# Kernel tuning notes

Measured on AMD Instinct MI355X. Metric: run time of the kernel, lower is better.

The kernel has to match this reference:

```python
import jax, jax.numpy as jnp
import numpy as np

N = 40000        # total nodes (2000 graphs x 20 nodes)
E = 60000        # edges per relation (before self-loops)
R = 6            # number of relations
IN = 32
HID = 128
OUT = 128
H = 2            # heads
C = 128          # per-head out channels (concat=False)
B = 2000         # number of graphs
NEG_SLOPE = 0.2


def setup_inputs() -> dict:
    key = jax.random.key(0)
    ks = jax.random.split(key, 16)
    rn = lambda k, s, sc=0.05: (jax.random.normal(k, s, jnp.float32) * sc)
    x = jax.random.normal(ks[0], (N, IN), jnp.float32)
    edge_index = jax.random.randint(ks[1], (R, 2, E), 0, N, dtype=jnp.int32)
    batch = (jnp.arange(N, dtype=jnp.int32) // (N // B)).astype(jnp.int32)
    return {
        "x": x, "edge_index": edge_index, "batch": batch,
        "Wl1": rn(ks[2], (R, IN, H * C)), "bl1": jnp.zeros((R, H * C), jnp.float32),
        "Wr1": rn(ks[3], (R, IN, H * C)), "br1": jnp.zeros((R, H * C), jnp.float32),
        "att1": rn(ks[4], (R, H, C)), "bias1": jnp.zeros((R, C), jnp.float32),
        "Wl2": rn(ks[5], (R, HID, H * C)), "bl2": jnp.zeros((R, H * C), jnp.float32),
        "Wr2": rn(ks[6], (R, HID, H * C)), "br2": jnp.zeros((R, H * C), jnp.float32),
        "att2": rn(ks[7], (R, H, C)), "bias2": jnp.zeros((R, C), jnp.float32),
        "ln1_g": jnp.ones((HID,), jnp.float32), "ln1_b": jnp.zeros((HID,), jnp.float32),
        "ln2_g": jnp.ones((HID,), jnp.float32), "ln2_b": jnp.zeros((HID,), jnp.float32),
        "query": rn(ks[8], (HID,), 0.02),
        "projW": rn(ks[9], (HID, OUT)), "projb": jnp.zeros((OUT,), jnp.float32),
    }


def _gatv2(x, src, dst, Wl, bl, Wr, br, att, bias):
    # x: [N, F]; src/dst: [Etot] (self-loops already appended)
    n = x.shape[0]
    xl = (x @ Wl + bl).reshape(n, H, C)   # source transform
    xr = (x @ Wr + br).reshape(n, H, C)   # target transform
    e = jax.nn.leaky_relu(xl[src] + xr[dst], NEG_SLOPE)   # [Etot, H, C]
    logits = jnp.einsum('ehc,hc->eh', e, att)             # [Etot, H]
    m = jax.ops.segment_max(logits, dst, num_segments=n)
    a = jnp.exp(logits - m[dst])
    s = jax.ops.segment_sum(a, dst, num_segments=n)
    w = a / s[dst]                                        # segment softmax
    out = jax.ops.segment_sum(w[:, :, None] * xl[src], dst, num_segments=n)
    return out.mean(axis=1) + bias                        # head-average (concat=False)


def _hetero_layer(x, edge_index, Wl, bl, Wr, br, att, bias):
    loops = jnp.broadcast_to(jnp.arange(N, dtype=edge_index.dtype), (R, N))
    src = jnp.concatenate([edge_index[:, 0, :], loops], axis=1)  # [R, E+N]
    dst = jnp.concatenate([edge_index[:, 1, :], loops], axis=1)
    outs = jax.vmap(_gatv2, in_axes=(None, 0, 0, 0, 0, 0, 0, 0, 0))(
        x, src, dst, Wl, bl, Wr, br, att, bias)
    return outs.sum(axis=0)  # HeteroConv aggr='sum'


def _layernorm(x, g, b, eps=1e-5):
    mu = x.mean(-1, keepdims=True)
    var = ((x - mu) ** 2).mean(-1, keepdims=True)
    return (x - mu) * jax.lax.rsqrt(var + eps) * g + b


def reference(x, edge_index, batch, Wl1, bl1, Wr1, br1, att1, bias1,
              Wl2, bl2, Wr2, br2, att2, bias2,
              ln1_g, ln1_b, ln2_g, ln2_b, query, projW, projb):
    h = _hetero_layer(x, edge_index, Wl1, bl1, Wr1, br1, att1, bias1)
    h = _layernorm(jnp.tanh(h), ln1_g, ln1_b)
    h = _hetero_layer(h, edge_index, Wl2, bl2, Wr2, br2, att2, bias2)
    h = _layernorm(jnp.tanh(h), ln2_g, ln2_b)
    # attention pooling over graphs (segment softmax on batch ids)
    scores = h @ query                              # [N]
    m = jax.ops.segment_max(scores, batch, num_segments=B)
    a = jnp.exp(scores - m[batch])
    s = jax.ops.segment_sum(a, batch, num_segments=B)
    w = a / s[batch]
    g = jax.ops.segment_sum(w[:, None] * h, batch, num_segments=B)  # [B, HID]
    return g @ projW + projb
```

## Files before the change

kernel.cpp:

```cpp
#include <hip/hip_runtime.h>
#include <math.h>

#define N_NODES 40000
#define E_EDGES 60000
#define R_REL 6
#define IN_F 32
#define HID_F 128
#define B_GRAPHS 2000
#define NODES_PER_G 20
#define NEG_SLOPE 0.2f

typedef __bf16 bf16x8 __attribute__((ext_vector_type(8)));
typedef float f32x4 __attribute__((ext_vector_type(4)));

__device__ __forceinline__ unsigned f2bfbits(float f) {
    unsigned u = __builtin_bit_cast(unsigned, f);
    return (u + 0x7FFFu + ((u >> 16) & 1u)) >> 16;
}
__device__ __forceinline__ float bflo(unsigned u) { return __builtin_bit_cast(float, u << 16); }
__device__ __forceinline__ float bfhi(unsigned u) { return __builtin_bit_cast(float, u & 0xFFFF0000u); }

__global__ __launch_bounds__(256) void build_links_kernel(
    const int* __restrict__ ei, int* __restrict__ head, int* __restrict__ nxt)
{
    int idx = blockIdx.x * 256 + threadIdx.x;
    if (idx >= R_REL * E_EDGES) return;
    int r = idx / E_EDGES;
    int e = idx - r * E_EDGES;
    int dst = ei[(size_t)r * 2 * E_EDGES + E_EDGES + e];
    int old = atomicExch(&head[r * N_NODES + dst], e);
    nxt[(size_t)r * E_EDGES + e] = old;
}

__global__ __launch_bounds__(256) void cvt_bf16_kernel(
    const float* __restrict__ src, unsigned* __restrict__ dst, int npairs)
{
    int i = blockIdx.x * 256 + threadIdx.x;
    if (i >= npairs) return;
    float2 v = *(const float2*)(src + 2 * i);
    dst[i] = f2bfbits(v.x) | (f2bfbits(v.y) << 16);
}

__global__ __launch_bounds__(256) void prep_w_kernel(
    const float* __restrict__ Wl, const float* __restrict__ Wr,
    const float* __restrict__ bl, const float* __restrict__ br,
    unsigned short* __restrict__ Bt, float* __restrict__ bcat, int K)
{
    int idx = blockIdx.x * 256 + threadIdx.x;
    if (idx >= R_REL * 512 * K) return;
    int k = idx % K;
    int rn = idx / K;
    int n = rn % 512;
    int r = rn / 512;
    int nn = n & 255;
    const float* W = (n < 256) ? Wl : Wr;
    float w = W[((size_t)r * K + k) * 256 + nn];
    Bt[idx] = (unsigned short)f2bfbits(w);
    if (k == 0)
        bcat[rn] = (n < 256) ? bl[r * 256 + nn] : br[r * 256 + nn];
}

template <int K>
__global__ __launch_bounds__(256) void gemm_mfma_kernel(
    const unsigned short* __restrict__ A,
    const unsigned short* __restrict__ BtAll,
    const float* __restrict__ biasAll,
    unsigned short* __restrict__ CAll)
{
    __shared__ char lds[16384];
    char* ldsA = lds;
    char* ldsB = lds + 8192;
    const unsigned short* Bt = BtAll + (size_t)blockIdx.z * 512 * K;
    const float* bias = biasAll + blockIdx.z * 512;
    unsigned short* C = CAll + (size_t)blockIdx.z * N_NODES * 512;
    int tid = threadIdx.x;
    int lane = tid & 63, wave = tid >> 6;
    int l16 = lane & 15, quad = lane >> 4;
    int wm = (wave >> 1) * 64, wn = (wave & 1) * 64;
    int m0 = blockIdx.x * 128;
    int n0 = blockIdx.y * 128;

    f32x4 acc[4][4] = {};

    for (int k0 = 0; k0 < K; k0 += 32) {
#pragma unroll
        for (int j = 0; j < 2; j++) {
            int o = wave * 2048 + j * 1024;
            int boff = o + lane * 16;
            int row = boff >> 6, ko = boff & 63;
            int gr = m0 + row;
            gr = gr < N_NODES ? gr : (N_NODES - 1);
            const char* gpA = (const char*)A + (size_t)gr * (K * 2) + k0 * 2 + ko;
            __builtin_amdgcn_global_load_lds(
                (const __attribute__((address_space(1))) void*)gpA,
                (__attribute__((address_space(3))) void*)(ldsA + o), 16, 0, 0);
            const char* gpB = (const char*)Bt + (size_t)(n0 + row) * (K * 2) + k0 * 2 + ko;
            __builtin_amdgcn_global_load_lds(
                (const __attribute__((address_space(1))) void*)gpB,
                (__attribute__((address_space(3))) void*)(ldsB + o), 16, 0, 0);
        }
        __syncthreads();
        bf16x8 af[4], bfr[4];
#pragma unroll
        for (int i = 0; i < 4; i++)
            af[i] = *(const bf16x8*)(ldsA + (wm + i * 16 + l16) * 64 + quad * 16);
#pragma unroll
        for (int j = 0; j < 4; j++)
            bfr[j] = *(const bf16x8*)(ldsB + (wn + j * 16 + l16) * 64 + quad * 16);
#pragma unroll
        for (int i = 0; i < 4; i++)
#pragma unroll
            for (int j = 0; j < 4; j++)
                acc[i][j] = __builtin_amdgcn_mfma_f32_16x16x32_bf16(af[i], bfr[j], acc[i][j], 0, 0, 0);
        __syncthreads();
    }

    float biasj[4];
#pragma unroll
    for (int j = 0; j < 4; j++) biasj[j] = bias[n0 + wn + j * 16 + l16];
#pragma unroll
    for (int i = 0; i < 4; i++) {
        int gr0 = m0 + wm + i * 16 + quad * 4;
#pragma unroll
        for (int j = 0; j < 4; j++) {
            int col = n0 + wn + j * 16 + l16;
#pragma unroll
            for (int rg = 0; rg < 4; rg++) {
                float a = acc[i][j][rg] + biasj[j];
                float b = __shfl_xor(a, 1);
                int grow = gr0 + rg;
                if (!(lane & 1) && grow < N_NODES) {
                    unsigned u = f2bfbits(a) | (f2bfbits(b) << 16);
                    *(unsigned*)((char*)C + ((size_t)grow * 512 + col) * 2) = u;
                }
            }
        }
    }
}

__global__ __launch_bounds__(256) void gat6_ln_kernel(
    const unsigned short* __restrict__ XLR,
    const int* __restrict__ head,
    const int* __restrict__ nxt,
    const int* __restrict__ ei,
    const float* __restrict__ att,
    const float* __restrict__ bias,
    const float* __restrict__ lng, const float* __restrict__ lnb,
    unsigned* __restrict__ hout)
{
    int gtid = blockIdx.x * 256 + threadIdx.x;
    int d = gtid >> 6;
    int lane = threadIdx.x & 63;
    if (d >= N_NODES) return;
    int hl = lane & 31;

    float tot0 = 0.f, tot1 = 0.f, tot2 = 0.f, tot3 = 0.f;
#pragma unroll 1
    for (int r = 0; r < R_REL; r++) {
        const char* base = (const char*)XLR + (size_t)r * N_NODES * 1024;
        const unsigned* xrp = (const unsigned*)(base + (size_t)d * 1024 + 512 + lane * 8);
        unsigned xu0 = xrp[0], xu1 = xrp[1];
        float xr0 = bflo(xu0), xr1 = bfhi(xu0), xr2 = bflo(xu1), xr3 = bfhi(xu1);
        float4 av = *(const float4*)(att + r * 256 + lane * 4);

        float s = 0.f, a0 = 0.f, a1 = 0.f, a2 = 0.f, a3 = 0.f;
        const int* srcs = ei + (size_t)r * 2 * E_EDGES;
        const int* nx = nxt + (size_t)r * E_EDGES;
        int e = head[r * N_NODES + d];
        int src = d;
        while (true) {
            const unsigned* xlp = (const unsigned*)(base + (size_t)src * 1024 + lane * 8);
            unsigned u0 = xlp[0], u1 = xlp[1];
            float xl0 = bflo(u0), xl1 = bfhi(u0), xl2 = bflo(u1), xl3 = bfhi(u1);
            float t0 = xl0 + xr0, t1 = xl1 + xr1, t2 = xl2 + xr2, t3 = xl3 + xr3;
            t0 = fmaxf(t0, NEG_SLOPE * t0);
            t1 = fmaxf(t1, NEG_SLOPE * t1);
            t2 = fmaxf(t2, NEG_SLOPE * t2);
            t3 = fmaxf(t3, NEG_SLOPE * t3);
            float p = t0 * av.x + t1 * av.y + t2 * av.z + t3 * av.w;
            p += __shfl_xor(p, 16);
            p += __shfl_xor(p, 8);
            p += __shfl_xor(p, 4);
            p += __shfl_xor(p, 2);
            p += __shfl_xor(p, 1);
            float w = __expf(fminf(p, 60.f));
            s += w;
            a0 = fmaf(w, xl0, a0);
            a1 = fmaf(w, xl1, a1);
            a2 = fmaf(w, xl2, a2);
            a3 = fmaf(w, xl3, a3);
            if (e < 0) break;
            src = srcs[e];
            e = nx[e];
        }
        float rs = 0.5f * __builtin_amdgcn_rcpf(s);
        float o0 = a0 * rs, o1 = a1 * rs, o2 = a2 * rs, o3 = a3 * rs;
        o0 += __shfl_xor(o0, 32);
        o1 += __shfl_xor(o1, 32);
        o2 += __shfl_xor(o2, 32);
        o3 += __shfl_xor(o3, 32);
        float4 bv = *(const float4*)(bias + r * 128 + hl * 4);
        tot0 += o0 + bv.x;
        tot1 += o1 + bv.y;
        tot2 += o2 + bv.z;
        tot3 += o3 + bv.w;
    }
    float v0 = tanhf(tot0), v1 = tanhf(tot1), v2 = tanhf(tot2), v3 = tanhf(tot3);
    float sum = v0 + v1 + v2 + v3;
    float sq = v0 * v0 + v1 * v1 + v2 * v2 + v3 * v3;
#pragma unroll
    for (int off = 16; off >= 1; off >>= 1) {
        sum += __shfl_xor(sum, off);
        sq  += __shfl_xor(sq, off);
    }
    float mean = sum * (1.f / 128.f);
    float var = sq * (1.f / 128.f) - mean * mean;
    float rstd = rsqrtf(var + 1e-5f);
    float4 gg = *(const float4*)(lng + hl * 4);
    float4 bb = *(const float4*)(lnb + hl * 4);
    float o0 = (v0 - mean) * rstd * gg.x + bb.x;
    float o1 = (v1 - mean) * rstd * gg.y + bb.y;
    float o2 = (v2 - mean) * rstd * gg.z + bb.z;
    float o3 = (v3 - mean) * rstd * gg.w + bb.w;
    if (lane < 32) {
        uint2 q;
        q.x = f2bfbits(o0) | (f2bfbits(o1) << 16);
        q.y = f2bfbits(o2) | (f2bfbits(o3) << 16);
        *((uint2*)(hout + (size_t)d * 64) + hl) = q;
    }
}

__global__ __launch_bounds__(256) void pool_kernel(
    const unsigned* __restrict__ hb, const float* __restrict__ query,
    float* __restrict__ gout)
{
    int gtid = blockIdx.x * 256 + threadIdx.x;
    int bg = gtid >> 6;
    int lane = threadIdx.x & 63;
    if (bg >= B_GRAPHS) return;
    float2 q = *(const float2*)(query + 2 * lane);
    float mx = -1e30f, ssum = 0.f, g0 = 0.f, g1 = 0.f;
    for (int i = 0; i < NODES_PER_G; i++) {
        unsigned u = hb[(size_t)(bg * NODES_PER_G + i) * 64 + lane];
        float h0 = bflo(u), h1 = bfhi(u);
        float p = h0 * q.x + h1 * q.y;
#pragma unroll
        for (int off = 32; off >= 1; off >>= 1) p += __shfl_xor(p, off, 64);
        float mn = fmaxf(mx, p);
        float sc = __expf(mx - mn), w = __expf(p - mn);
        ssum = ssum * sc + w;
        g0 = g0 * sc + w * h0;
        g1 = g1 * sc + w * h1;
        mx = mn;
    }
    float2 o; o.x = g0 / ssum; o.y = g1 / ssum;
    *(float2*)(gout + (size_t)bg * 128 + 2 * lane) = o;
}

__global__ __launch_bounds__(128) void proj_kernel(
    const float* __restrict__ g, const float* __restrict__ W,
    const float* __restrict__ bias, float* __restrict__ out)
{
    int bg = blockIdx.x;
    int o = threadIdx.x;
    const float* gp = g + (size_t)bg * 128;
    float acc = bias[o];
    for (int k = 0; k < 128; k++) acc = fmaf(gp[k], W[k * 128 + o], acc);
    out[(size_t)bg * 128 + o] = acc;
}

extern "C" void kernel_launch(void* const* d_in, const int* in_sizes, int n_in,
                              void* d_out, int out_size, void* d_ws, size_t ws_size,
                              hipStream_t stream)
{
    const float* x     = (const float*)d_in[0];
    const int*   ei    = (const int*)d_in[1];
    const float* Wl1   = (const float*)d_in[3];
    const float* bl1   = (const float*)d_in[4];
    const float* Wr1   = (const float*)d_in[5];
    const float* br1   = (const float*)d_in[6];
    const float* att1  = (const float*)d_in[7];
    const float* bias1 = (const float*)d_in[8];
    const float* Wl2   = (const float*)d_in[9];
    const float* bl2   = (const float*)d_in[10];
    const float* Wr2   = (const float*)d_in[11];
    const float* br2   = (const float*)d_in[12];
    const float* att2  = (const float*)d_in[13];
    const float* bias2 = (const float*)d_in[14];
    const float* ln1g  = (const float*)d_in[15];
    const float* ln1b  = (const float*)d_in[16];
    const float* ln2g  = (const float*)d_in[17];
    const float* ln2b  = (const float*)d_in[18];
    const float* query = (const float*)d_in[19];
    const float* projW = (const float*)d_in[20];
    const float* projb = (const float*)d_in[21];
    float* out = (float*)d_out;

    unsigned short* xlr6 = (unsigned short*)d_ws;
    unsigned short* h1bf = xlr6 + (size_t)R_REL * N_NODES * 512;
    unsigned short* xbf  = h1bf + (size_t)N_NODES * 128;
    unsigned short* Bt1  = xbf + (size_t)N_NODES * 32;
    unsigned short* Bt2  = Bt1 + R_REL * 512 * 32;
    float* bc1  = (float*)(Bt2 + R_REL * 512 * 128);
    float* bc2  = bc1 + R_REL * 512;
    float* gb   = bc2 + R_REL * 512;
    int* headp  = (int*)(gb + (size_t)B_GRAPHS * 128);
    int* nextp  = headp + R_REL * N_NODES;

    hipMemsetAsync(headp, 0xFF, sizeof(int) * R_REL * N_NODES, stream);
    build_links_kernel<<<(R_REL * E_EDGES + 255) / 256, 256, 0, stream>>>(ei, headp, nextp);
    cvt_bf16_kernel<<<(N_NODES * 16 + 255) / 256, 256, 0, stream>>>(x, (unsigned*)xbf, N_NODES * 16);
    prep_w_kernel<<<(R_REL * 512 * 32 + 255) / 256, 256, 0, stream>>>(Wl1, Wr1, bl1, br1, Bt1, bc1, 32);
    prep_w_kernel<<<(R_REL * 512 * 128 + 255) / 256, 256, 0, stream>>>(Wl2, Wr2, bl2, br2, Bt2, bc2, 128);

    dim3 ggrid((N_NODES + 127) / 128, 4, R_REL);
    gemm_mfma_kernel<32><<<ggrid, 256, 0, stream>>>(xbf, Bt1, bc1, xlr6);
    gat6_ln_kernel<<<N_NODES / 4, 256, 0, stream>>>(
        xlr6, headp, nextp, ei, att1, bias1, ln1g, ln1b, (unsigned*)h1bf);
    gemm_mfma_kernel<128><<<ggrid, 256, 0, stream>>>(h1bf, Bt2, bc2, xlr6);
    gat6_ln_kernel<<<N_NODES / 4, 256, 0, stream>>>(
        xlr6, headp, nextp, ei, att2, bias2, ln2g, ln2b, (unsigned*)h1bf);
    pool_kernel<<<B_GRAPHS / 4, 256, 0, stream>>>((unsigned*)h1bf, query, gb);
    proj_kernel<<<B_GRAPHS, 128, 0, stream>>>(gb, projW, projb, out);
}
```

Before: 497.6 us.

## Replace linked-list edge traversal with CSR built by count-scan-scatter, unroll by two

Swaps the atomicExch linked-list adjacency for a CSR layout built with a histogram, a three-stage prefix scan and an atomic scatter, with self-loops included as explicit entries. The GAT kernel then walks a contiguous range of source ids, removing the dependent pointer-chasing loads (src, next). It also processes two edges per iteration with separate accumulators to expose more memory-level parallelism. The cost is four extra small kernel launches for CSR construction, and edge order within a row is nondeterministic, so float summation order varies from run to run.

```diff
diff --git a/kernel.cpp b/kernel.cpp
--- a/kernel.cpp
+++ b/kernel.cpp
@@ -9,6 +9,9 @@
 #define B_GRAPHS 2000
 #define NODES_PER_G 20
 #define NEG_SLOPE 0.2f
+#define NB (R_REL * N_NODES)
+#define NTOT (R_REL * (E_EDGES + N_NODES))
+#define NBLK ((NB + 255) / 256)
 
 typedef __bf16 bf16x8 __attribute__((ext_vector_type(8)));
 typedef float f32x4 __attribute__((ext_vector_type(4)));
@@ -20,16 +23,89 @@
 __device__ __forceinline__ float bflo(unsigned u) { return __builtin_bit_cast(float, u << 16); }
 __device__ __forceinline__ float bfhi(unsigned u) { return __builtin_bit_cast(float, u & 0xFFFF0000u); }
 
-__global__ __launch_bounds__(256) void build_links_kernel(
-    const int* __restrict__ ei, int* __restrict__ head, int* __restrict__ nxt)
+__global__ __launch_bounds__(256) void count_kernel(
+    const int* __restrict__ ei, int* __restrict__ cnt)
 {
     int idx = blockIdx.x * 256 + threadIdx.x;
-    if (idx >= R_REL * E_EDGES) return;
-    int r = idx / E_EDGES;
-    int e = idx - r * E_EDGES;
-    int dst = ei[(size_t)r * 2 * E_EDGES + E_EDGES + e];
-    int old = atomicExch(&head[r * N_NODES + dst], e);
-    nxt[(size_t)r * E_EDGES + e] = old;
+    if (idx >= NTOT) return;
+    int bin;
+    if (idx < R_REL * E_EDGES) {
+        int r = idx / E_EDGES, e = idx - r * E_EDGES;
+        bin = r * N_NODES + ei[(size_t)r * 2 * E_EDGES + E_EDGES + e];
+    } else {
+        bin = idx - R_REL * E_EDGES;
+    }
+    atomicAdd(&cnt[bin], 1);
+}
+
+__global__ __launch_bounds__(256) void scan1_kernel(
+    const int* __restrict__ cnt, int* __restrict__ part, int* __restrict__ bsum)
+{
+    int i = blockIdx.x * 256 + threadIdx.x;
+    int v = (i < NB) ? cnt[i] : 0;
+    int lane = threadIdx.x & 63, w = threadIdx.x >> 6;
+    int x = v;
+#pragma unroll
+    for (int off = 1; off < 64; off <<= 1) {
+        int y = __shfl_up(x, off, 64);
+        if (lane >= off) x += y;
+    }
+    __shared__ int ws[4];
+    if (lane == 63) ws[w] = x;
+    __syncthreads();
+    int add = 0;
+    for (int j = 0; j < w; j++) add += ws[j];
+    int incl = x + add;
+    if (i < NB) part[i] = incl - v;
+    if (threadIdx.x == 255) bsum[blockIdx.x] = incl;
+}
+
+__global__ __launch_bounds__(1024) void scan2_kernel(
+    const int* __restrict__ bsum, int* __restrict__ boff)
+{
+    __shared__ int buf[1024];
+    int t = threadIdx.x;
+    int v0 = (t < NBLK) ? bsum[t] : 0;
+    buf[t] = v0;
+    __syncthreads();
+    for (int off = 1; off < 1024; off <<= 1) {
+        int v = (t >= off) ? buf[t - off] : 0;
+        __syncthreads();
+        buf[t] += v;
+        __syncthreads();
+    }
+    if (t < NBLK) boff[t] = buf[t] - v0;
+}
+
+__global__ __launch_bounds__(256) void scan3_kernel(
+    const int* __restrict__ part, const int* __restrict__ boff,
+    int* __restrict__ rowptr, int* __restrict__ cursor)
+{
+    int i = blockIdx.x * 256 + threadIdx.x;
+    if (i < NB) {
+        int v = part[i] + boff[i >> 8];
+        rowptr[i] = v;
+        cursor[i] = v;
+    }
+    if (i == 0) rowptr[NB] = NTOT;
+}
+
+__global__ __launch_bounds__(256) void scatter_kernel(
+    const int* __restrict__ ei, int* __restrict__ cursor, int* __restrict__ csr)
+{
+    int idx = blockIdx.x * 256 + threadIdx.x;
+    if (idx >= NTOT) return;
+    int bin, src;
+    if (idx < R_REL * E_EDGES) {
+        int r = idx / E_EDGES, e = idx - r * E_EDGES;
+        src = ei[(size_t)r * 2 * E_EDGES + e];
+        bin = r * N_NODES + ei[(size_t)r * 2 * E_EDGES + E_EDGES + e];
+    } else {
+        bin = idx - R_REL * E_EDGES;
+        src = bin % N_NODES;
+    }
+    int pos = atomicAdd(&cursor[bin], 1);
+    csr[pos] = src;
 }
 
 __global__ __launch_bounds__(256) void cvt_bf16_kernel(
@@ -140,9 +216,8 @@
 
 __global__ __launch_bounds__(256) void gat6_ln_kernel(
     const unsigned short* __restrict__ XLR,
-    const int* __restrict__ head,
-    const int* __restrict__ nxt,
-    const int* __restrict__ ei,
+    const int* __restrict__ rowptr,
+    const int* __restrict__ csr,
     const float* __restrict__ att,
     const float* __restrict__ bias,
     const float* __restrict__ lng, const float* __restrict__ lnb,
@@ -163,37 +238,67 @@
         float xr0 = bflo(xu0), xr1 = bfhi(xu0), xr2 = bflo(xu1), xr3 = bfhi(xu1);
         float4 av = *(const float4*)(att + r * 256 + lane * 4);
 
-        float s = 0.f, a0 = 0.f, a1 = 0.f, a2 = 0.f, a3 = 0.f;
-        const int* srcs = ei + (size_t)r * 2 * E_EDGES;
-        const int* nx = nxt + (size_t)r * E_EDGES;
-        int e = head[r * N_NODES + d];
-        int src = d;
-        while (true) {
-            const unsigned* xlp = (const unsigned*)(base + (size_t)src * 1024 + lane * 8);
-            unsigned u0 = xlp[0], u1 = xlp[1];
-            float xl0 = bflo(u0), xl1 = bfhi(u0), xl2 = bflo(u1), xl3 = bfhi(u1);
-            float t0 = xl0 + xr0, t1 = xl1 + xr1, t2 = xl2 + xr2, t3 = xl3 + xr3;
-            t0 = fmaxf(t0, NEG_SLOPE * t0);
-            t1 = fmaxf(t1, NEG_SLOPE * t1);
-            t2 = fmaxf(t2, NEG_SLOPE * t2);
-            t3 = fmaxf(t3, NEG_SLOPE * t3);
-            float p = t0 * av.x + t1 * av.y + t2 * av.z + t3 * av.w;
-            p += __shfl_xor(p, 16);
-            p += __shfl_xor(p, 8);
-            p += __shfl_xor(p, 4);
-            p += __shfl_xor(p, 2);
-            p += __shfl_xor(p, 1);
-            float w = __expf(fminf(p, 60.f));
-            s += w;
-            a0 = fmaf(w, xl0, a0);
-            a1 = fmaf(w, xl1, a1);
-            a2 = fmaf(w, xl2, a2);
-            a3 = fmaf(w, xl3, a3);
-            if (e < 0) break;
-            src = srcs[e];
-            e = nx[e];
+        int bin = r * N_NODES + d;
+        int beg = __builtin_amdgcn_readfirstlane(rowptr[bin]);
+        int end = __builtin_amdgcn_readfirstlane(rowptr[bin + 1]);
+
+        float sA = 0.f, a0 = 0.f, a1 = 0.f, a2 = 0.f, a3 = 0.f;
+        float sB = 0.f, b0 = 0.f, b1 = 0.f, b2 = 0.f, b3 = 0.f;
+        int i = beg;
+        for (; i + 2 <= end; i += 2) {
+            int s0 = csr[i], s1 = csr[i + 1];
+            const unsigned* pA = (const unsigned*)(base + (size_t)s0 * 1024 + lane * 8);
+            const unsigned* pB = (const unsigned*)(base + (size_t)s1 * 1024 + lane * 8);
+            unsigned uA0 = pA[0], uA1 = pA[1];
+            unsigned uB0 = pB[0], uB1 = pB[1];
+            float xA0 = bflo(uA0), xA1 = bfhi(uA0), xA2 = bflo(uA1), xA3 = bfhi(uA1);
+            float xB0 = bflo(uB0), xB1 = bfhi(uB0), xB2 = bflo(uB1), xB3 = bfhi(uB1);
+            float tA0 = xA0 + xr0, tA1 = xA1 + xr1, tA2 = xA2 + xr2, tA3 = xA3 + xr3;
+            float tB0 = xB0 + xr0, tB1 = xB1 + xr1, tB2 = xB2 + xr2, tB3 = xB3 + xr3;
+            tA0 = fmaxf(tA0, NEG_SLOPE * tA0); tB0 = fmaxf(tB0, NEG_SLOPE * tB0);
+            tA1 = fmaxf(tA1, NEG_SLOPE * tA1); tB1 = fmaxf(tB1, NEG_SLOPE * tB1);
+            tA2 = fmaxf(tA2, NEG_SLOPE * tA2); tB2 = fmaxf(tB2, NEG_SLOPE * tB2);
+            tA3 = fmaxf(tA3, NEG_SLOPE * tA3); tB3 = fmaxf(tB3, NEG_SLOPE * tB3);
+            float pa = tA0 * av.x + tA1 * av.y + tA2 * av.z + tA3 * av.w;
+            float pb = tB0 * av.x + tB1 * av.y + tB2 * av.z + tB3 * av.w;
+            pa += __shfl_xor(pa, 16); pb += __shfl_xor(pb, 16);
+            pa += __shfl_xor(pa, 8);  pb += __shfl_xor(pb, 8);
+            pa += __shfl_xor(pa, 4);  pb += __shfl_xor(pb, 4);
+            pa += __shfl_xor(pa, 2);  pb += __shfl_xor(pb, 2);
+            pa += __shfl_xor(pa, 1);  pb += __shfl_xor(pb, 1);
+            float wa = __expf(fminf(pa, 60.f));
+            float wb = __expf(fminf(pb, 60.f));
+            sA += wa; sB += wb;
+            a0 = fmaf(wa, xA0, a0); b0 = fmaf(wb, xB0, b0);
+            a1 = fmaf(wa, xA1, a1); b1 = fmaf(wb, xB1, b1);
+            a2 = fmaf(wa, xA2, a2); b2 = fmaf(wb, xB2, b2);
+            a3 = fmaf(wa, xA3, a3); b3 = fmaf(wb, xB3, b3);
         }
-        float rs = 0.5f * __builtin_amdgcn_rcpf(s);
+        if (i < end) {
+            int s0 = csr[i];
+            const unsigned* pA = (const unsigned*)(base + (size_t)s0 * 1024 + lane * 8);
+            unsigned uA0 = pA[0], uA1 = pA[1];
+            float xA0 = bflo(uA0), xA1 = bfhi(uA0), xA2 = bflo(uA1), xA3 = bfhi(uA1);
+            float tA0 = xA0 + xr0, tA1 = xA1 + xr1, tA2 = xA2 + xr2, tA3 = xA3 + xr3;
+            tA0 = fmaxf(tA0, NEG_SLOPE * tA0);
+            tA1 = fmaxf(tA1, NEG_SLOPE * tA1);
+            tA2 = fmaxf(tA2, NEG_SLOPE * tA2);
+            tA3 = fmaxf(tA3, NEG_SLOPE * tA3);
+            float pa = tA0 * av.x + tA1 * av.y + tA2 * av.z + tA3 * av.w;
+            pa += __shfl_xor(pa, 16);
+            pa += __shfl_xor(pa, 8);
+            pa += __shfl_xor(pa, 4);
+            pa += __shfl_xor(pa, 2);
+            pa += __shfl_xor(pa, 1);
+            float wa = __expf(fminf(pa, 60.f));
+            sA += wa;
+            a0 = fmaf(wa, xA0, a0);
+            a1 = fmaf(wa, xA1, a1);
+            a2 = fmaf(wa, xA2, a2);
+            a3 = fmaf(wa, xA3, a3);
+        }
+        sA += sB; a0 += b0; a1 += b1; a2 += b2; a3 += b3;
+        float rs = 0.5f * __builtin_amdgcn_rcpf(sA);
         float o0 = a0 * rs, o1 = a1 * rs, o2 = a2 * rs, o3 = a3 * rs;
         o0 += __shfl_xor(o0, 32);
         o1 += __shfl_xor(o1, 32);
@@ -304,11 +409,21 @@
     float* bc1  = (float*)(Bt2 + R_REL * 512 * 128);
     float* bc2  = bc1 + R_REL * 512;
     float* gb   = bc2 + R_REL * 512;
-    int* headp  = (int*)(gb + (size_t)B_GRAPHS * 128);
-    int* nextp  = headp + R_REL * N_NODES;
-
-    hipMemsetAsync(headp, 0xFF, sizeof(int) * R_REL * N_NODES, stream);
-    build_links_kernel<<<(R_REL * E_EDGES + 255) / 256, 256, 0, stream>>>(ei, headp, nextp);
+    int* cnt    = (int*)(gb + (size_t)B_GRAPHS * 128);
+    int* part   = cnt + NB;
+    int* rowptr = part + NB;
+    int* cursor = rowptr + NB + 1;
+    int* bsum   = cursor + NB;
+    int* boff   = bsum + NBLK;
+    int* csr    = boff + NBLK;
+
+    hipMemsetAsync(cnt, 0, sizeof(int) * NB, stream);
+    count_kernel<<<(NTOT + 255) / 256, 256, 0, stream>>>(ei, cnt);
+    scan1_kernel<<<NBLK, 256, 0, stream>>>(cnt, part, bsum);
+    scan2_kernel<<<1, 1024, 0, stream>>>(bsum, boff);
+    scan3_kernel<<<NBLK, 256, 0, stream>>>(part, boff, rowptr, cursor);
+    scatter_kernel<<<(NTOT + 255) / 256, 256, 0, stream>>>(ei, cursor, csr);
+
     cvt_bf16_kernel<<<(N_NODES * 16 + 255) / 256, 256, 0, stream>>>(x, (unsigned*)xbf, N_NODES * 16);
     prep_w_kernel<<<(R_REL * 512 * 32 + 255) / 256, 256, 0, stream>>>(Wl1, Wr1, bl1, br1, Bt1, bc1, 32);
     prep_w_kernel<<<(R_REL * 512 * 128 + 255) / 256, 256, 0, stream>>>(Wl2, Wr2, bl2, br2, Bt2, bc2, 128);
@@ -316,10 +431,10 @@
     dim3 ggrid((N_NODES + 127) / 128, 4, R_REL);
     gemm_mfma_kernel<32><<<ggrid, 256, 0, stream>>>(xbf, Bt1, bc1, xlr6);
     gat6_ln_kernel<<<N_NODES / 4, 256, 0, stream>>>(
-        xlr6, headp, nextp, ei, att1, bias1, ln1g, ln1b, (unsigned*)h1bf);
+        xlr6, rowptr, csr, att1, bias1, ln1g, ln1b, (unsigned*)h1bf);
     gemm_mfma_kernel<128><<<ggrid, 256, 0, stream>>>(h1bf, Bt2, bc2, xlr6);
     gat6_ln_kernel<<<N_NODES / 4, 256, 0, stream>>>(
-        xlr6, headp, nextp, ei, att2, bias2, ln2g, ln2b, (unsigned*)h1bf);
+        xlr6, rowptr, csr, att2, bias2, ln2g, ln2b, (unsigned*)h1bf);
     pool_kernel<<<B_GRAPHS / 4, 256, 0, stream>>>((unsigned*)h1bf, query, gb);
     proj_kernel<<<B_GRAPHS, 128, 0, stream>>>(gb, projW, projb, out);
 }
```

Measured after the change: 481.5 us. -3.2%, faster.
